# Kernel tuning notes

Measured on AMD Instinct MI355X. Metric: run time of the kernel, lower is better.

The kernel has to match this reference:

```python
import jax, jax.numpy as jnp
import numpy as np

DECAY = 0.999
EPS = 1e-05
COMMITMENT_COST = 0.25
M, D = 1024, 256
B, H, W = 32, 32, 32


def setup_inputs() -> dict:
    key = jax.random.key(0)
    k1, k2 = jax.random.split(key)
    init_bound = 1.0 / M
    x = jax.random.normal(k1, (B, H, W, D), dtype=jnp.float32)
    embedding = jax.random.uniform(k2, (M, D), dtype=jnp.float32,
                                   minval=-init_bound, maxval=init_bound)
    ema_count = jnp.zeros((M,), dtype=jnp.float32)
    ema_weight = embedding  # buffer initialized as embedding.clone()
    return {"x": x, "embedding": embedding, "ema_count": ema_count,
            "ema_weight": ema_weight}


def reference(x, embedding, ema_count, ema_weight):
    Mn, Dn = embedding.shape
    x_flat = jax.lax.stop_gradient(x).reshape(-1, Dn)          # [N, D]
    N = x_flat.shape[0]

    # (-cdist)^2 == squared euclidean distance; argmin is the same.
    x_sq = jnp.sum(x_flat * x_flat, axis=-1, keepdims=True)    # [N, 1]
    e_sq = jnp.sum(embedding * embedding, axis=-1)             # [M]
    distances = x_sq - 2.0 * (x_flat @ embedding.T) + e_sq[None, :]  # [N, M]
    indices = jnp.argmin(distances, axis=-1)                   # [N]

    quantized = embedding[indices].reshape(x.shape)            # gather

    # one-hot column sums == scatter-add of ones; encodings.T @ x_flat == scatter-add rows
    counts = jnp.zeros((Mn,), x.dtype).at[indices].add(1.0)    # [M]
    dw = jnp.zeros((Mn, Dn), x.dtype).at[indices].add(x_flat)  # [M, D]

    new_count = DECAY * ema_count + (1.0 - DECAY) * counts
    n = jnp.sum(new_count)
    new_count = (new_count + EPS) / (n + Mn * EPS) * n
    new_weight = DECAY * ema_weight + (1.0 - DECAY) * dw
    new_embedding = new_weight / new_count[:, None]

    codebook_loss = jnp.mean((jax.lax.stop_gradient(x) - quantized) ** 2)
    e_latent_loss = jnp.mean((x - jax.lax.stop_gradient(quantized)) ** 2)
    commitment_loss = COMMITMENT_COST * e_latent_loss

    quantized_st = x + jax.lax.stop_gradient(quantized - x)    # straight-through

    avg_probs = counts / N
    perplexity = jnp.exp(-jnp.sum(avg_probs * jnp.log(avg_probs + 1e-10)))

    return (quantized_st, commitment_loss, codebook_loss, perplexity,
            new_embedding, new_count, new_weight)
```

## Files before the change

kernel.cpp:

```cpp
#include <hip/hip_runtime.h>
#include <cfloat>
#include <math.h>

#define N_TOK 32768
#define DIM   256
#define MCODE 1024

typedef unsigned short u16;
typedef unsigned long long u64;
typedef __attribute__((ext_vector_type(8))) short short8;
typedef __attribute__((ext_vector_type(4))) float f32x4;

constexpr float DECAY_ = 0.999f;
constexpr float OMD_   = (float)(1.0 - 0.999);
constexpr float EPS_   = 1e-5f;
constexpr float MEPS_  = (float)(1024 * 1e-5);

constexpr int WS_EH   = 0;
constexpr int WS_EL   = 131072;
constexpr int WS_ESQ  = 262144;
constexpr int WS_CNTI = 263168;
constexpr int WS_BI   = 264192;
constexpr int WS_LP   = 296960;
constexpr int WS_KEY  = 299008;

constexpr int OUT_Q        = 0;
constexpr int OUT_COMMIT   = 8388608;
constexpr int OUT_CODEBOOK = 8388609;
constexpr int OUT_PERP     = 8388610;
constexpr int OUT_NE       = 8388611;
constexpr int OUT_NC       = 8650755;
constexpr int OUT_NW       = 8651779;

static __device__ __forceinline__ u16 f2bf(float f) {
    unsigned u = __float_as_uint(f);
    unsigned r = (u + 0x7fff + ((u >> 16) & 1)) >> 16;
    return (u16)r;
}
static __device__ __forceinline__ float bf2f(u16 h) {
    return __uint_as_float(((unsigned)h) << 16);
}
static __device__ __forceinline__ void gl2lds16(const u16* g, char* l) {
    __builtin_amdgcn_global_load_lds(
        (const __attribute__((address_space(1))) unsigned int*)g,
        (__attribute__((address_space(3))) unsigned int*)l, 16, 0, 0);
}
static __device__ __forceinline__ unsigned fmap(float f) {
    unsigned u = __float_as_uint(f);
    return (u & 0x80000000u) ? ~u : (u | 0x80000000u);
}

static __device__ __forceinline__ void load_row8(const float* __restrict__ src,
                                                 int wave_id, int lane,
                                                 float* vv, size_t* o) {
    int rb = wave_id >> 6, kc = (wave_id >> 3) & 7, t = wave_id & 7;
    int row = rb * 128 + t * 16 + (lane & 15);
    int k   = kc * 32 + (lane >> 4) * 8;
    const float* s = &src[row * DIM + k];
    float4 v0 = *(const float4*)s, v1 = *(const float4*)(s + 4);
    vv[0]=v0.x; vv[1]=v0.y; vv[2]=v0.z; vv[3]=v0.w;
    vv[4]=v1.x; vv[5]=v1.y; vv[6]=v1.z; vv[7]=v1.w;
    *o = (size_t)wave_id * 512 + lane * 8;
}
static __device__ __forceinline__ void pack_wave_hi(const float* __restrict__ src,
                                                    u16* __restrict__ dh,
                                                    int wave_id, int lane) {
    float vv[8]; size_t o;
    load_row8(src, wave_id, lane, vv, &o);
    short8 hv;
#pragma unroll
    for (int j = 0; j < 8; ++j) hv[j] = (short)f2bf(vv[j]);
    *(short8*)&dh[o] = hv;
}
static __device__ __forceinline__ void pack_wave_hl(const float* __restrict__ src,
                                                    u16* __restrict__ dh,
                                                    u16* __restrict__ dl,
                                                    int wave_id, int lane) {
    float vv[8]; size_t o;
    load_row8(src, wave_id, lane, vv, &o);
    short8 hv, lv;
#pragma unroll
    for (int j = 0; j < 8; ++j) {
        u16 h = f2bf(vv[j]);
        hv[j] = (short)h;
        lv[j] = (short)f2bf(vv[j] - bf2f(h));
    }
    *(short8*)&dh[o] = hv;
    *(short8*)&dl[o] = lv;
}

__global__ __launch_bounds__(256) void vq_setup(const float* __restrict__ x,
                                                const float* __restrict__ emb,
                                                u16* __restrict__ xh,
                                                u16* __restrict__ eh,
                                                u16* __restrict__ el,
                                                float* __restrict__ esq,
                                                u64* __restrict__ keys,
                                                int* __restrict__ cnti) {
    const int b = blockIdx.x, tid = threadIdx.x;
    const int lane = tid & 63, w = tid >> 6;
    if (b < 4096) { pack_wave_hi(x, xh, b * 4 + w, lane); return; }
    const int p = b - 4096;
    if (p < 128) {
        pack_wave_hl(emb, eh, el, p * 4 + w, lane);
    } else if (p < 384) {
        int c = (p - 128) * 4 + w;
        float4 v = *(const float4*)&emb[c * DIM + lane * 4];
        float s = v.x * v.x + v.y * v.y + v.z * v.z + v.w * v.w;
#pragma unroll
        for (int off = 32; off; off >>= 1) s += __shfl_xor(s, off, 64);
        if (lane == 0) esq[c] = s;
    } else if (p < 512) {
        keys[(p - 384) * 256 + tid] = ~0ULL;
    } else {
#pragma unroll
        for (int i = 0; i < 4; ++i) cnti[i * 256 + tid] = 0;
    }
}

__global__ __launch_bounds__(256) void vq_scores_mfma(const u16* __restrict__ xh,
                                                      const u16* __restrict__ eh,
                                                      const u16* __restrict__ el,
                                                      const float* __restrict__ esq,
                                                      u64* __restrict__ keys) {
    __shared__ __align__(16) char smem[33792];
    const int tid  = threadIdx.x;
    const int lane = tid & 63, w = tid >> 6;
    const int wm = w & 1, wn = w >> 1;
    const int raw = blockIdx.x;
    const int rb = (raw >> 6) * 8 + (raw & 7);
    const int cs = (raw >> 3) & 7;

    const u16* gb0 = xh + (size_t)rb * 32768;
    const u16* gb1 = eh + (size_t)cs * 32768;
    const u16* gb2 = el + (size_t)cs * 32768;

    const short8* Ah = (const short8*)(smem);
    const short8* Bh = (const short8*)(smem + 8192);
    const short8* Bl = (const short8*)(smem + 16384);

    f32x4 acc[4][4];
#pragma unroll
    for (int i = 0; i < 4; ++i)
#pragma unroll
        for (int j = 0; j < 4; ++j) acc[i][j] = (f32x4)0.f;

    for (int kc = 0; kc < 8; ++kc) {
        __syncthreads();
#pragma unroll
        for (int j = 0; j < 6; ++j) {
            int t = w * 6 + j;
            int arr = t >> 3, slot = t & 7;
            const u16* g = (arr == 0 ? gb0 : (arr == 1 ? gb1 : gb2))
                           + kc * 4096 + slot * 512 + lane * 8;
            gl2lds16(g, smem + arr * 8192 + slot * 1024);
        }
        __syncthreads();

        short8 ah[4];
#pragma unroll
        for (int tm = 0; tm < 4; ++tm)
            ah[tm] = Ah[(wm * 4 + tm) * 64 + lane];
#pragma unroll
        for (int tn = 0; tn < 4; ++tn) {
            int bidx = (wn * 4 + tn) * 64 + lane;
            short8 bh = Bh[bidx], bl = Bl[bidx];
#pragma unroll
            for (int tm = 0; tm < 4; ++tm) {
                acc[tm][tn] = __builtin_amdgcn_mfma_f32_16x16x32_bf16(ah[tm], bh, acc[tm][tn], 0, 0, 0);
                acc[tm][tn] = __builtin_amdgcn_mfma_f32_16x16x32_bf16(ah[tm], bl, acc[tm][tn], 0, 0, 0);
            }
        }
    }

    __syncthreads();
    float* cv = (float*)smem;
    int*   ci = (int*)(smem + 16896);
    const int ln = lane & 15, quad = lane >> 4;
#pragma unroll
    for (int tm = 0; tm < 4; ++tm) {
        float bv[4];
        int   bi[4];
#pragma unroll
        for (int r = 0; r < 4; ++r) { bv[r] = FLT_MAX; bi[r] = 0; }
#pragma unroll
        for (int tn = 0; tn < 4; ++tn) {
            int c = cs * 128 + wn * 64 + tn * 16 + ln;
            float ec = esq[c];
#pragma unroll
            for (int r = 0; r < 4; ++r) {
                float d = fmaf(-2.f, acc[tm][tn][r], ec);
                if (d < bv[r]) { bv[r] = d; bi[r] = c; }
            }
        }
        int row0 = wm * 64 + tm * 16 + quad * 4;
        int slot = wn * 16 + ln;
#pragma unroll
        for (int r = 0; r < 4; ++r) {
            cv[(row0 + r) * 33 + slot] = bv[r];
            ci[(row0 + r) * 33 + slot] = bi[r];
        }
    }
    __syncthreads();
    if (tid < 128) {
        float bv = cv[tid * 33];
        int   bi = ci[tid * 33];
#pragma unroll
        for (int s = 1; s < 32; ++s) {
            float v = cv[tid * 33 + s];
            int  ix = ci[tid * 33 + s];
            if (v < bv || (v == bv && ix < bi)) { bv = v; bi = ix; }
        }
        u64 key = ((u64)fmap(bv) << 32) | (unsigned)bi;
        atomicMin(&keys[rb * 128 + tid], key);
    }
}

__global__ __launch_bounds__(256) void vq_quant(const float* __restrict__ x,
                                                const float* __restrict__ emb,
                                                const u64* __restrict__ keys,
                                                float* __restrict__ outq,
                                                int* __restrict__ cnti,
                                                int* __restrict__ bi_arr,
                                                float* __restrict__ lpart) {
    const int tid = threadIdx.x, lane = tid & 63, w = tid >> 6;
    const float4* x4 = (const float4*)x;
    const float4* e4 = (const float4*)emb;
    float4* o4 = (float4*)outq;
    float lacc = 0.f;
#pragma unroll
    for (int it = 0; it < 4; ++it) {
        int row = blockIdx.x * 16 + it * 4 + w;
        int bi = (int)(unsigned)(keys[row] & 0xffffffffULL);
        if (lane == 0) { atomicAdd(&cnti[bi], 1); bi_arr[row] = bi; }
        float4 xv = x4[row * 64 + lane];
        float4 ev = e4[bi * 64 + lane];
        float4 q;
        q.x = xv.x + (ev.x - xv.x);  q.y = xv.y + (ev.y - xv.y);
        q.z = xv.z + (ev.z - xv.z);  q.w = xv.w + (ev.w - xv.w);
        o4[row * 64 + lane] = q;
        float dx = xv.x - ev.x, dy = xv.y - ev.y, dz = xv.z - ev.z, dwv = xv.w - ev.w;
        lacc += dx * dx + dy * dy + dz * dz + dwv * dwv;
    }
#pragma unroll
    for (int off = 32; off; off >>= 1) lacc += __shfl_xor(lacc, off, 64);
    __shared__ float red[4];
    if (lane == 0) red[w] = lacc;
    __syncthreads();
    if (tid == 0) lpart[blockIdx.x] = red[0] + red[1] + red[2] + red[3];
}

#define MEGA_CAP 6144
__global__ __launch_bounds__(256) void vq_mega(const float* __restrict__ x,
                                               const float* __restrict__ ema_count,
                                               const float* __restrict__ ema_weight,
                                               const int* __restrict__ cnti,
                                               const int* __restrict__ bi_arr,
                                               const float* __restrict__ lpart,
                                               float* __restrict__ out) {
    const int m = blockIdx.x, tid = threadIdx.x;
    __shared__ float fs[256];
    __shared__ int list[MEGA_CAP];
    __shared__ int lcount;

    float rsum = 0.f;
#pragma unroll
    for (int i = 0; i < 4; ++i) rsum += ema_count[tid * 4 + i];
    fs[tid] = rsum;
    if (tid == 0) lcount = 0;
    __syncthreads();
    for (int s = 128; s; s >>= 1) { if (tid < s) fs[tid] += fs[tid + s]; __syncthreads(); }
    const float n = DECAY_ * fs[0] + OMD_ * (float)N_TOK;
    __syncthreads();

    const int4* b4 = (const int4*)bi_arr;
#pragma unroll 4
    for (int i = tid; i < N_TOK / 4; i += 256) {
        int4 v = b4[i];
        if (v.x == m) { int p = atomicAdd(&lcount, 1); if (p < MEGA_CAP) list[p] = 4 * i; }
        if (v.y == m) { int p = atomicAdd(&lcount, 1); if (p < MEGA_CAP) list[p] = 4 * i + 1; }
        if (v.z == m) { int p = atomicAdd(&lcount, 1); if (p < MEGA_CAP) list[p] = 4 * i + 2; }
        if (v.w == m) { int p = atomicAdd(&lcount, 1); if (p < MEGA_CAP) list[p] = 4 * i + 3; }
    }
    __syncthreads();
    const int nm = lcount;
    float dwsum;
    if (nm <= MEGA_CAP) {
        float a0 = 0.f, a1 = 0.f, a2 = 0.f, a3 = 0.f;
        int i = 0;
        for (; i + 4 <= nm; i += 4) {
            a0 += x[list[i]     * DIM + tid];
            a1 += x[list[i + 1] * DIM + tid];
            a2 += x[list[i + 2] * DIM + tid];
            a3 += x[list[i + 3] * DIM + tid];
        }
        for (; i < nm; ++i) a0 += x[list[i] * DIM + tid];
        dwsum = (a0 + a1) + (a2 + a3);
    } else {
        __shared__ int chunk[256];
        float a0 = 0.f;
        for (int base = 0; base < N_TOK; base += 256) {
            __syncthreads();
            chunk[tid] = bi_arr[base + tid];
            __syncthreads();
            for (int j = 0; j < 256; ++j)
                if (chunk[j] == m) a0 += x[(base + j) * DIM + tid];
        }
        dwsum = a0;
    }

    float raw_m = DECAY_ * ema_count[m] + OMD_ * (float)nm;
    float ncm = (raw_m + EPS_) / (n + MEPS_) * n;
    float nw = DECAY_ * ema_weight[m * DIM + tid] + OMD_ * dwsum;
    out[OUT_NW + m * DIM + tid] = nw;
    out[OUT_NE + m * DIM + tid] = nw / ncm;
    if (tid == 0) out[OUT_NC + m] = ncm;

    if (m == 0) {
        float ent = 0.f;
#pragma unroll
        for (int i = 0; i < 4; ++i) {
            float p = (float)cnti[tid * 4 + i] / (float)N_TOK;
            ent += p * logf(p + 1e-10f);
        }
        __syncthreads();
        fs[tid] = ent;
        __syncthreads();
        for (int s = 128; s; s >>= 1) { if (tid < s) fs[tid] += fs[tid + s]; __syncthreads(); }
        float entr = fs[0];
        __syncthreads();
        float ls = 0.f;
#pragma unroll
        for (int k = 0; k < 8; ++k) ls += lpart[tid + 256 * k];
        fs[tid] = ls;
        __syncthreads();
        for (int s = 128; s; s >>= 1) { if (tid < s) fs[tid] += fs[tid + s]; __syncthreads(); }
        if (tid == 0) {
            float mean = fs[0] / (float)(N_TOK * DIM);
            out[OUT_COMMIT]   = 0.25f * mean;
            out[OUT_CODEBOOK] = mean;
            out[OUT_PERP]     = expf(-entr);
        }
    }
}

extern "C" void kernel_launch(void* const* d_in, const int* in_sizes, int n_in,
                              void* d_out, int out_size, void* d_ws, size_t ws_size,
                              hipStream_t stream) {
    const float* x          = (const float*)d_in[0];
    const float* emb        = (const float*)d_in[1];
    const float* ema_count  = (const float*)d_in[2];
    const float* ema_weight = (const float*)d_in[3];
    float* out = (float*)d_out;
    float* wf  = (float*)d_ws;

    u16* xh = (u16*)d_out;
    u16* eh = (u16*)(wf + WS_EH);
    u16* el = (u16*)(wf + WS_EL);

    float* esq    = wf + WS_ESQ;
    int*   cnti   = (int*)(wf + WS_CNTI);
    int*   bi_arr = (int*)(wf + WS_BI);
    float* lpart  = wf + WS_LP;
    u64*   keys   = (u64*)(wf + WS_KEY);

    vq_setup<<<4609, 256, 0, stream>>>(x, emb, xh, eh, el, esq, keys, cnti);
    vq_scores_mfma<<<2048, 256, 0, stream>>>(xh, eh, el, esq, keys);
    vq_quant<<<2048, 256, 0, stream>>>(x, emb, keys, out, cnti, bi_arr, lpart);
    vq_mega<<<MCODE, 256, 0, stream>>>(x, ema_count, ema_weight, cnti, bi_arr,
                                       lpart, out);
}
```

Before: 160.8 us.

## Fuse quantize and EMA-update kernels into one launch with atomic ticket finalization

```diff
diff --git a/kernel.cpp b/kernel.cpp
--- a/kernel.cpp
+++ b/kernel.cpp
@@ -19,10 +19,8 @@
 constexpr int WS_EH   = 0;
 constexpr int WS_EL   = 131072;
 constexpr int WS_ESQ  = 262144;
-constexpr int WS_CNTI = 263168;
-constexpr int WS_BI   = 264192;
-constexpr int WS_LP   = 296960;
-constexpr int WS_KEY  = 299008;
+constexpr int WS_KEY  = 263168;
+constexpr int WS_ACC  = 328704;
 
 constexpr int OUT_Q        = 0;
 constexpr int OUT_COMMIT   = 8388608;
@@ -96,7 +94,7 @@
                                                 u16* __restrict__ el,
                                                 float* __restrict__ esq,
                                                 u64* __restrict__ keys,
-                                                int* __restrict__ cnti) {
+                                                float* __restrict__ acc) {
     const int b = blockIdx.x, tid = threadIdx.x;
     const int lane = tid & 63, w = tid >> 6;
     if (b < 4096) { pack_wave_hi(x, xh, b * 4 + w, lane); return; }
@@ -113,8 +111,7 @@
     } else if (p < 512) {
         keys[(p - 384) * 256 + tid] = ~0ULL;
     } else {
-#pragma unroll
-        for (int i = 0; i < 4; ++i) cnti[i * 256 + tid] = 0;
+        if (tid < 8) acc[tid] = 0.f;
     }
 }
 
@@ -216,130 +213,120 @@
     }
 }
 
-__global__ __launch_bounds__(256) void vq_quant(const float* __restrict__ x,
+#define MEGA_CAP 6144
+__global__ __launch_bounds__(256) void vq_tail2(const float* __restrict__ x,
                                                 const float* __restrict__ emb,
+                                                const float* __restrict__ ema_count,
+                                                const float* __restrict__ ema_weight,
                                                 const u64* __restrict__ keys,
-                                                float* __restrict__ outq,
-                                                int* __restrict__ cnti,
-                                                int* __restrict__ bi_arr,
-                                                float* __restrict__ lpart) {
-    const int tid = threadIdx.x, lane = tid & 63, w = tid >> 6;
-    const float4* x4 = (const float4*)x;
-    const float4* e4 = (const float4*)emb;
-    float4* o4 = (float4*)outq;
-    float lacc = 0.f;
-#pragma unroll
-    for (int it = 0; it < 4; ++it) {
-        int row = blockIdx.x * 16 + it * 4 + w;
-        int bi = (int)(unsigned)(keys[row] & 0xffffffffULL);
-        if (lane == 0) { atomicAdd(&cnti[bi], 1); bi_arr[row] = bi; }
-        float4 xv = x4[row * 64 + lane];
-        float4 ev = e4[bi * 64 + lane];
-        float4 q;
-        q.x = xv.x + (ev.x - xv.x);  q.y = xv.y + (ev.y - xv.y);
-        q.z = xv.z + (ev.z - xv.z);  q.w = xv.w + (ev.w - xv.w);
-        o4[row * 64 + lane] = q;
-        float dx = xv.x - ev.x, dy = xv.y - ev.y, dz = xv.z - ev.z, dwv = xv.w - ev.w;
-        lacc += dx * dx + dy * dy + dz * dz + dwv * dwv;
-    }
-#pragma unroll
-    for (int off = 32; off; off >>= 1) lacc += __shfl_xor(lacc, off, 64);
-    __shared__ float red[4];
-    if (lane == 0) red[w] = lacc;
-    __syncthreads();
-    if (tid == 0) lpart[blockIdx.x] = red[0] + red[1] + red[2] + red[3];
-}
-
-#define MEGA_CAP 6144
-__global__ __launch_bounds__(256) void vq_mega(const float* __restrict__ x,
-                                               const float* __restrict__ ema_count,
-                                               const float* __restrict__ ema_weight,
-                                               const int* __restrict__ cnti,
-                                               const int* __restrict__ bi_arr,
-                                               const float* __restrict__ lpart,
-                                               float* __restrict__ out) {
-    const int m = blockIdx.x, tid = threadIdx.x;
+                                                float* __restrict__ out,
+                                                float* __restrict__ acc) {
+    const int b = blockIdx.x, tid = threadIdx.x;
+    float* loss_acc = acc;
+    float* ent_acc  = acc + 1;
+    unsigned* ticket = (unsigned*)(acc + 2);
     __shared__ float fs[256];
     __shared__ int list[MEGA_CAP];
     __shared__ int lcount;
 
-    float rsum = 0.f;
-#pragma unroll
-    for (int i = 0; i < 4; ++i) rsum += ema_count[tid * 4 + i];
-    fs[tid] = rsum;
-    if (tid == 0) lcount = 0;
+    if (b < 1024) {
+        const int m = b;
+        float rsum = 0.f;
+#pragma unroll
+        for (int i = 0; i < 4; ++i) rsum += ema_count[tid * 4 + i];
+        fs[tid] = rsum;
+        if (tid == 0) lcount = 0;
+        __syncthreads();
+        for (int s = 128; s; s >>= 1) { if (tid < s) fs[tid] += fs[tid + s]; __syncthreads(); }
+        const float n = DECAY_ * fs[0] + OMD_ * (float)N_TOK;
+        __syncthreads();
+
+        const ulonglong2* k2 = (const ulonglong2*)keys;
+#pragma unroll 4
+        for (int i = tid; i < N_TOK / 2; i += 256) {
+            ulonglong2 v = k2[i];
+            if ((unsigned)(v.x & 0xffffffffULL) == (unsigned)m) {
+                int p = atomicAdd(&lcount, 1); if (p < MEGA_CAP) list[p] = 2 * i;
+            }
+            if ((unsigned)(v.y & 0xffffffffULL) == (unsigned)m) {
+                int p = atomicAdd(&lcount, 1); if (p < MEGA_CAP) list[p] = 2 * i + 1;
+            }
+        }
+        __syncthreads();
+        const int nm = lcount;
+        float dwsum;
+        if (nm <= MEGA_CAP) {
+            float a0 = 0.f, a1 = 0.f, a2 = 0.f, a3 = 0.f;
+            int i = 0;
+            for (; i + 4 <= nm; i += 4) {
+                a0 += x[list[i]     * DIM + tid];
+                a1 += x[list[i + 1] * DIM + tid];
+                a2 += x[list[i + 2] * DIM + tid];
+                a3 += x[list[i + 3] * DIM + tid];
+            }
+            for (; i < nm; ++i) a0 += x[list[i] * DIM + tid];
+            dwsum = (a0 + a1) + (a2 + a3);
+        } else {
+            __shared__ int chunk[256];
+            float a0 = 0.f;
+            for (int base = 0; base < N_TOK; base += 256) {
+                __syncthreads();
+                chunk[tid] = (int)(unsigned)(keys[base + tid] & 0xffffffffULL);
+                __syncthreads();
+                for (int j = 0; j < 256; ++j)
+                    if (chunk[j] == m) a0 += x[(base + j) * DIM + tid];
+            }
+            dwsum = a0;
+        }
+
+        float raw_m = DECAY_ * ema_count[m] + OMD_ * (float)nm;
+        float ncm = (raw_m + EPS_) / (n + MEPS_) * n;
+        float nw = DECAY_ * ema_weight[m * DIM + tid] + OMD_ * dwsum;
+        out[OUT_NW + m * DIM + tid] = nw;
+        out[OUT_NE + m * DIM + tid] = nw / ncm;
+        if (tid == 0) {
+            out[OUT_NC + m] = ncm;
+            float p = (float)nm / (float)N_TOK;
+            atomicAdd(ent_acc, p * logf(p + 1e-10f));
+        }
+    } else {
+        const int lane = tid & 63, w = tid >> 6;
+        const float4* x4 = (const float4*)x;
+        const float4* e4 = (const float4*)emb;
+        float4* o4 = (float4*)out;
+        float lacc = 0.f;
+#pragma unroll
+        for (int it = 0; it < 4; ++it) {
+            int row = (b - 1024) * 16 + it * 4 + w;
+            int bi = (int)(unsigned)(keys[row] & 0xffffffffULL);
+            float4 xv = x4[row * 64 + lane];
+            float4 ev = e4[bi * 64 + lane];
+            float4 q;
+            q.x = xv.x + (ev.x - xv.x);  q.y = xv.y + (ev.y - xv.y);
+            q.z = xv.z + (ev.z - xv.z);  q.w = xv.w + (ev.w - xv.w);
+            o4[row * 64 + lane] = q;
+            float dx = xv.x - ev.x, dy = xv.y - ev.y;
+            float dz = xv.z - ev.z, dwv = xv.w - ev.w;
+            lacc += dx * dx + dy * dy + dz * dz + dwv * dwv;
+        }
+#pragma unroll
+        for (int off = 32; off; off >>= 1) lacc += __shfl_xor(lacc, off, 64);
+        if (lane == 0) fs[w] = lacc;
+        __syncthreads();
+        if (tid == 0) atomicAdd(loss_acc, fs[0] + fs[1] + fs[2] + fs[3]);
+    }
+
     __syncthreads();
-    for (int s = 128; s; s >>= 1) { if (tid < s) fs[tid] += fs[tid + s]; __syncthreads(); }
-    const float n = DECAY_ * fs[0] + OMD_ * (float)N_TOK;
-    __syncthreads();
-
-    const int4* b4 = (const int4*)bi_arr;
-#pragma unroll 4
-    for (int i = tid; i < N_TOK / 4; i += 256) {
-        int4 v = b4[i];
-        if (v.x == m) { int p = atomicAdd(&lcount, 1); if (p < MEGA_CAP) list[p] = 4 * i; }
-        if (v.y == m) { int p = atomicAdd(&lcount, 1); if (p < MEGA_CAP) list[p] = 4 * i + 1; }
-        if (v.z == m) { int p = atomicAdd(&lcount, 1); if (p < MEGA_CAP) list[p] = 4 * i + 2; }
-        if (v.w == m) { int p = atomicAdd(&lcount, 1); if (p < MEGA_CAP) list[p] = 4 * i + 3; }
-    }
-    __syncthreads();
-    const int nm = lcount;
-    float dwsum;
-    if (nm <= MEGA_CAP) {
-        float a0 = 0.f, a1 = 0.f, a2 = 0.f, a3 = 0.f;
-        int i = 0;
-        for (; i + 4 <= nm; i += 4) {
-            a0 += x[list[i]     * DIM + tid];
-            a1 += x[list[i + 1] * DIM + tid];
-            a2 += x[list[i + 2] * DIM + tid];
-            a3 += x[list[i + 3] * DIM + tid];
-        }
-        for (; i < nm; ++i) a0 += x[list[i] * DIM + tid];
-        dwsum = (a0 + a1) + (a2 + a3);
-    } else {
-        __shared__ int chunk[256];
-        float a0 = 0.f;
-        for (int base = 0; base < N_TOK; base += 256) {
-            __syncthreads();
-            chunk[tid] = bi_arr[base + tid];
-            __syncthreads();
-            for (int j = 0; j < 256; ++j)
-                if (chunk[j] == m) a0 += x[(base + j) * DIM + tid];
-        }
-        dwsum = a0;
-    }
-
-    float raw_m = DECAY_ * ema_count[m] + OMD_ * (float)nm;
-    float ncm = (raw_m + EPS_) / (n + MEPS_) * n;
-    float nw = DECAY_ * ema_weight[m * DIM + tid] + OMD_ * dwsum;
-    out[OUT_NW + m * DIM + tid] = nw;
-    out[OUT_NE + m * DIM + tid] = nw / ncm;
-    if (tid == 0) out[OUT_NC + m] = ncm;
-
-    if (m == 0) {
-        float ent = 0.f;
-#pragma unroll
-        for (int i = 0; i < 4; ++i) {
-            float p = (float)cnti[tid * 4 + i] / (float)N_TOK;
-            ent += p * logf(p + 1e-10f);
-        }
-        __syncthreads();
-        fs[tid] = ent;
-        __syncthreads();
-        for (int s = 128; s; s >>= 1) { if (tid < s) fs[tid] += fs[tid + s]; __syncthreads(); }
-        float entr = fs[0];
-        __syncthreads();
-        float ls = 0.f;
-#pragma unroll
-        for (int k = 0; k < 8; ++k) ls += lpart[tid + 256 * k];
-        fs[tid] = ls;
-        __syncthreads();
-        for (int s = 128; s; s >>= 1) { if (tid < s) fs[tid] += fs[tid + s]; __syncthreads(); }
-        if (tid == 0) {
-            float mean = fs[0] / (float)(N_TOK * DIM);
+    __threadfence();
+    if (tid == 0) {
+        unsigned t = atomicAdd(ticket, 1u);
+        if (t == 3071u) {
+            float ls  = atomicAdd(loss_acc, 0.f);
+            float ent = atomicAdd(ent_acc, 0.f);
+            float mean = ls / (float)(N_TOK * DIM);
             out[OUT_COMMIT]   = 0.25f * mean;
             out[OUT_CODEBOOK] = mean;
-            out[OUT_PERP]     = expf(-entr);
+            out[OUT_PERP]     = expf(-ent);
         }
     }
 }
@@ -358,15 +345,12 @@
     u16* eh = (u16*)(wf + WS_EH);
     u16* el = (u16*)(wf + WS_EL);
 
-    float* esq    = wf + WS_ESQ;
-    int*   cnti   = (int*)(wf + WS_CNTI);
-    int*   bi_arr = (int*)(wf + WS_BI);
-    float* lpart  = wf + WS_LP;
-    u64*   keys   = (u64*)(wf + WS_KEY);
-
-    vq_setup<<<4609, 256, 0, stream>>>(x, emb, xh, eh, el, esq, keys, cnti);
+    float* esq = wf + WS_ESQ;
+    u64*   keys = (u64*)(wf + WS_KEY);
+    float* acc  = wf + WS_ACC;
+
+    vq_setup<<<4609, 256, 0, stream>>>(x, emb, xh, eh, el, esq, keys, acc);
     vq_scores_mfma<<<2048, 256, 0, stream>>>(xh, eh, el, esq, keys);
-    vq_quant<<<2048, 256, 0, stream>>>(x, emb, keys, out, cnti, bi_arr, lpart);
-    vq_mega<<<MCODE, 256, 0, stream>>>(x, ema_count, ema_weight, cnti, bi_arr,
-                                       lpart, out);
-}
+    vq_tail2<<<3072, 256, 0, stream>>>(x, emb, ema_count, ema_weight, keys,
+                                       out, acc);
+}
```

After: 427.4 us. 2.66x slower.
